# Kernel optimization log

Hardware: AMD Instinct MI355X
Metric: run time of the kernel (lower is better)

## Reference

```python
import jax, jax.numpy as jnp
import numpy as np

SEQ, B, IN, H = 512, 64, 256, 512

def _lin_params(key, out_d, in_d):
    k1, k2 = jax.random.split(key)
    bound = 1.0 / np.sqrt(in_d)
    w = jax.random.uniform(k1, (out_d, in_d), jnp.float32, -bound, bound)
    b = jax.random.uniform(k2, (out_d,), jnp.float32, -bound, bound)
    return w, b

def setup_inputs() -> dict:
    key = jax.random.key(0)
    ks = jax.random.split(key, 9)
    x = jax.random.normal(ks[0], (SEQ, B, IN), jnp.float32)
    h0 = jnp.zeros((B, H), jnp.float32)
    c0 = jnp.zeros((B, H), jnp.float32)
    Wf_w, Wf_b = _lin_params(ks[1], H, IN)
    Uf_w, Uf_b = _lin_params(ks[2], H, H)
    Wi_w, Wi_b = _lin_params(ks[3], H, IN)
    Ui_w, Ui_b = _lin_params(ks[4], H, H)
    Wo_w, Wo_b = _lin_params(ks[5], H, IN)
    Uo_w, Uo_b = _lin_params(ks[6], H, H)
    Wc_w, Wc_b = _lin_params(ks[7], H, IN)
    Uc_w, Uc_b = _lin_params(ks[8], H, H)
    return dict(x=x, h0=h0, c0=c0,
                Wf_w=Wf_w, Wf_b=Wf_b, Uf_w=Uf_w, Uf_b=Uf_b,
                Wi_w=Wi_w, Wi_b=Wi_b, Ui_w=Ui_w, Ui_b=Ui_b,
                Wo_w=Wo_w, Wo_b=Wo_b, Uo_w=Uo_w, Uo_b=Uo_b,
                Wc_w=Wc_w, Wc_b=Wc_b, Uc_w=Uc_w, Uc_b=Uc_b)

def reference(x, h0, c0,
              Wf_w, Wf_b, Uf_w, Uf_b,
              Wi_w, Wi_b, Ui_w, Ui_b,
              Wo_w, Wo_b, Uo_w, Uo_b,
              Wc_w, Wc_b, Uc_w, Uc_b):
    # Precompute all input-to-hidden projections in one batched GEMM per gate.
    xf = jnp.einsum('tbi,hi->tbh', x, Wf_w) + Wf_b  # (T,B,H)
    xi = jnp.einsum('tbi,hi->tbh', x, Wi_w) + Wi_b
    xo = jnp.einsum('tbi,hi->tbh', x, Wo_w) + Wo_b
    xc = jnp.einsum('tbi,hi->tbh', x, Wc_w) + Wc_b

    def step(carry, xs):
        h, c = carry
        xft, xit, xot, xct = xs
        f = jax.nn.sigmoid(xft + h @ Uf_w.T + Uf_b)
        i = jax.nn.sigmoid(xit + h @ Ui_w.T + Ui_b)
        o = jax.nn.sigmoid(xot + h @ Uo_w.T + Uo_b)
        c = f * c + i * jnp.tanh(xct + h @ Uc_w.T + Uc_b)
        h = o * jnp.tanh(c)
        return (h, c), h

    (h, c), h_seq = jax.lax.scan(step, (h0, c0), (xf, xi, xo, xc))
    return h_seq, h, c
```

## Files before the change

### kernel.cpp

```cpp
#include <hip/hip_runtime.h>


#define T_STEPS 512
#define BATCH   64
#define IN_D    256
#define HID     512
#define NGROUP  4
#define NSLICE  16
#define BLK_B   16
#define BLK_H   32
#define THREADS 512

using short8  = __attribute__((ext_vector_type(8))) short;
using float4v = __attribute__((ext_vector_type(4))) float;

#define FRAG_ADDR(f) (((f) << 4) + (((f) >> 4) << 4))

__device__ __forceinline__ unsigned short f2bf(float f) {
    union { float f; unsigned int i; } v; v.f = f;
    unsigned int r = v.i + 0x7fff + ((v.i >> 16) & 1);
    return (unsigned short)(r >> 16);
}
__device__ __forceinline__ short8 pack8(float4 a, float4 b) {
    short8 s;
    s[0]=(short)f2bf(a.x); s[1]=(short)f2bf(a.y); s[2]=(short)f2bf(a.z); s[3]=(short)f2bf(a.w);
    s[4]=(short)f2bf(b.x); s[5]=(short)f2bf(b.y); s[6]=(short)f2bf(b.z); s[7]=(short)f2bf(b.w);
    return s;
}
__device__ __forceinline__ float sigm(float v) { return 1.0f / (1.0f + __expf(-v)); }
__device__ __forceinline__ float tanh_(float v) { return 2.0f / (1.0f + __expf(-2.0f * v)) - 1.0f; }

__global__ __launch_bounds__(256, 1) void lstm_init_flags(unsigned int* flags, int n) {
    int i = blockIdx.x * blockDim.x + threadIdx.x;
    if (i < n) flags[i] = 0u;
}

__global__ __launch_bounds__(THREADS, 2) void lstm_persist(
    const float* __restrict__ x,
    const float* __restrict__ h0,
    const float* __restrict__ c0,
    const float* __restrict__ Wf, const float* __restrict__ Wfb,
    const float* __restrict__ Uf, const float* __restrict__ Ufb,
    const float* __restrict__ Wi, const float* __restrict__ Wib,
    const float* __restrict__ Ui, const float* __restrict__ Uib,
    const float* __restrict__ Wo, const float* __restrict__ Wob,
    const float* __restrict__ Uo, const float* __restrict__ Uob,
    const float* __restrict__ Wc, const float* __restrict__ Wcb,
    const float* __restrict__ Uc, const float* __restrict__ Ucb,
    float* out,
    unsigned int* flags)
{
    __shared__ __attribute__((aligned(16))) unsigned char hfrag[17392];
    __shared__ __attribute__((aligned(16))) unsigned char xfrag[8688];
    __shared__ float g_lds[8 * 256];

    const int tid  = threadIdx.x;
    const int lane = tid & 63;
    const int wave = tid >> 6;
    const int gate = wave >> 1;
    const int hlf  = wave & 1;
    const int grp  = blockIdx.x & 3;
    const int slc  = blockIdx.x >> 2;
    const int bb   = grp * BLK_B;
    const int hbase= slc * BLK_H;
    const int lm   = lane & 15;
    const int lq   = lane >> 4;
    const int row  = tid >> 5;
    const int seg  = tid & 31;

    const float* Ug  = (gate == 0) ? Uf : (gate == 1) ? Ui : (gate == 2) ? Uo : Uc;
    const float* Wg  = (gate == 0) ? Wf : (gate == 1) ? Wi : (gate == 2) ? Wo : Wc;
    const float* Wbg = (gate == 0) ? Wfb : (gate == 1) ? Wib : (gate == 2) ? Wob : Wcb;
    const float* Ubg = (gate == 0) ? Ufb : (gate == 1) ? Uib : (gate == 2) ? Uob : Ucb;
    const int ng = hbase + hlf * 16 + lm;

    short8 ufrag[16];
#pragma unroll
    for (int ks = 0; ks < 16; ++ks) {
        const float* p = Ug + (size_t)ng * HID + ks * 32 + lq * 8;
        ufrag[ks] = pack8(*(const float4*)(p), *(const float4*)(p + 4));
    }
    short8 wfrag[8];
#pragma unroll
    for (int ks = 0; ks < 8; ++ks) {
        const float* p = Wg + (size_t)ng * IN_D + ks * 32 + lq * 8;
        wfrag[ks] = pack8(*(const float4*)(p), *(const float4*)(p + 4));
    }
    const float bias = Wbg[ng] + Ubg[ng];

    float c_reg = c0[(size_t)(bb + row) * HID + hbase + seg];

    {
        const float* ph = h0 + (size_t)(bb + row) * HID + seg * 16;
        int f0 = (seg >> 1) * 64 + (seg & 1) * 32 + row;
        *(short8*)(hfrag + FRAG_ADDR(f0))      = pack8(*(const float4*)(ph),     *(const float4*)(ph + 4));
        *(short8*)(hfrag + FRAG_ADDR(f0 + 16)) = pack8(*(const float4*)(ph + 8), *(const float4*)(ph + 12));

        const float* px = x + (size_t)(bb + row) * IN_D + seg * 8;
        int fx = (seg >> 2) * 64 + (seg & 3) * 16 + row;
        *(short8*)(xfrag + FRAG_ADDR(fx)) = pack8(*(const float4*)(px), *(const float4*)(px + 4));
    }
    float4 xn0, xn1;
    {
        const float* px = x + ((size_t)1 * BATCH + bb + row) * IN_D + seg * 8;
        xn0 = *(const float4*)(px); xn1 = *(const float4*)(px + 4);
    }
    __syncthreads();

    float4v accx0 = {bias, bias, bias, bias};
    float4v accx1 = {0.f, 0.f, 0.f, 0.f};
#pragma unroll
    for (int ks = 0; ks < 8; ++ks) {
        short8 a = *(const short8*)(xfrag + FRAG_ADDR(ks * 64 + lane));
        if (ks & 1) accx1 = __builtin_amdgcn_mfma_f32_16x16x32_bf16(a, wfrag[ks], accx1, 0, 0, 0);
        else        accx0 = __builtin_amdgcn_mfma_f32_16x16x32_bf16(a, wfrag[ks], accx0, 0, 0, 0);
    }

    unsigned int* const cnt = flags + (size_t)grp * T_STEPS;
    float* const out_h = out + (size_t)T_STEPS * BATCH * HID;
    float* const out_c = out_h + (size_t)BATCH * HID;

    for (int t = 0; t < T_STEPS; ++t) {
        float4v acc0 = accx0, acc1 = accx1;
#pragma unroll
        for (int ks = 0; ks < 16; ++ks) {
            short8 a = *(const short8*)(hfrag + FRAG_ADDR(ks * 64 + lane));
            if (ks & 1) acc1 = __builtin_amdgcn_mfma_f32_16x16x32_bf16(a, ufrag[ks], acc1, 0, 0, 0);
            else        acc0 = __builtin_amdgcn_mfma_f32_16x16x32_bf16(a, ufrag[ks], acc0, 0, 0, 0);
        }
        float4v acc = acc0 + acc1;
#pragma unroll
        for (int r = 0; r < 4; ++r)
            g_lds[wave * 256 + (lq * 4 + r) * 16 + lm] = acc[r];
        __syncthreads();

        float hv;
        {
            int hf2 = seg >> 4, nn = seg & 15;
            float fpre = g_lds[(0 * 2 + hf2) * 256 + row * 16 + nn];
            float ipre = g_lds[(1 * 2 + hf2) * 256 + row * 16 + nn];
            float opre = g_lds[(2 * 2 + hf2) * 256 + row * 16 + nn];
            float gpre = g_lds[(3 * 2 + hf2) * 256 + row * 16 + nn];
            float fv = sigm(fpre), iv = sigm(ipre), ov = sigm(opre);
            float gv = tanh_(gpre);
            c_reg = fv * c_reg + iv * gv;
            hv = ov * tanh_(c_reg);
        }
        __hip_atomic_store(out + ((size_t)t * BATCH + bb + row) * HID + hbase + seg,
                           hv, __ATOMIC_RELAXED, __HIP_MEMORY_SCOPE_AGENT);
        if (t == T_STEPS - 1) {
            out_h[(size_t)(bb + row) * HID + hbase + seg] = hv;
            out_c[(size_t)(bb + row) * HID + hbase + seg] = c_reg;
        }

        if (t + 1 < T_STEPS) {
            int fx = (seg >> 2) * 64 + (seg & 3) * 16 + row;
            *(short8*)(xfrag + FRAG_ADDR(fx)) = pack8(xn0, xn1);
            int tn = (t + 2 < T_STEPS) ? (t + 2) : (T_STEPS - 1);
            const float* px = x + ((size_t)tn * BATCH + bb + row) * IN_D + seg * 8;
            xn0 = *(const float4*)(px); xn1 = *(const float4*)(px + 4);
        }

        asm volatile("s_waitcnt vmcnt(0)" ::: "memory");
        __syncthreads();

        if (t + 1 < T_STEPS) {
            if (tid == 0)
                __hip_atomic_fetch_add(&cnt[t], 1u, __ATOMIC_RELAXED, __HIP_MEMORY_SCOPE_AGENT);

            accx0 = (float4v){bias, bias, bias, bias};
            accx1 = (float4v){0.f, 0.f, 0.f, 0.f};
#pragma unroll
            for (int ks = 0; ks < 8; ++ks) {
                short8 a = *(const short8*)(xfrag + FRAG_ADDR(ks * 64 + lane));
                if (ks & 1) accx1 = __builtin_amdgcn_mfma_f32_16x16x32_bf16(a, wfrag[ks], accx1, 0, 0, 0);
                else        accx0 = __builtin_amdgcn_mfma_f32_16x16x32_bf16(a, wfrag[ks], accx0, 0, 0, 0);
            }

            if (tid == 0) {
                while (__hip_atomic_load(&cnt[t], __ATOMIC_RELAXED, __HIP_MEMORY_SCOPE_AGENT)
                       < (unsigned)NSLICE) {  }
            }
            __syncthreads();

            {
                const float* src = out + ((size_t)t * BATCH + bb + row) * HID + seg * 16;
                float4 a0 = *(const float4*)(src);
                float4 a1 = *(const float4*)(src + 4);
                float4 a2 = *(const float4*)(src + 8);
                float4 a3 = *(const float4*)(src + 12);
                int f0 = (seg >> 1) * 64 + (seg & 1) * 32 + row;
                *(short8*)(hfrag + FRAG_ADDR(f0))      = pack8(a0, a1);
                *(short8*)(hfrag + FRAG_ADDR(f0 + 16)) = pack8(a2, a3);
            }
            __syncthreads();
        }
    }
}

extern "C" void kernel_launch(void* const* d_in, const int* in_sizes, int n_in,
                              void* d_out, int out_size, void* d_ws, size_t ws_size,
                              hipStream_t stream) {
    (void)in_sizes; (void)n_in; (void)out_size; (void)ws_size;
    const float* x   = (const float*)d_in[0];
    const float* h0  = (const float*)d_in[1];
    const float* c0  = (const float*)d_in[2];
    const float* Wf  = (const float*)d_in[3];
    const float* Wfb = (const float*)d_in[4];
    const float* Uf  = (const float*)d_in[5];
    const float* Ufb = (const float*)d_in[6];
    const float* Wi  = (const float*)d_in[7];
    const float* Wib = (const float*)d_in[8];
    const float* Ui  = (const float*)d_in[9];
    const float* Uib = (const float*)d_in[10];
    const float* Wo  = (const float*)d_in[11];
    const float* Wob = (const float*)d_in[12];
    const float* Uo  = (const float*)d_in[13];
    const float* Uob = (const float*)d_in[14];
    const float* Wc  = (const float*)d_in[15];
    const float* Wcb = (const float*)d_in[16];
    const float* Uc  = (const float*)d_in[17];
    const float* Ucb = (const float*)d_in[18];

    unsigned int* flags = (unsigned int*)d_ws;
    const int nflags = NGROUP * T_STEPS;

    lstm_init_flags<<<(nflags + 255) / 256, 256, 0, stream>>>(flags, nflags);
    lstm_persist<<<NGROUP * NSLICE, THREADS, 0, stream>>>(
        x, h0, c0,
        Wf, Wfb, Uf, Ufb, Wi, Wib, Ui, Uib,
        Wo, Wob, Uo, Uob, Wc, Wcb, Uc, Ucb,
        (float*)d_out, flags);
}
```

Before: 1.570 ms.

## Replace counter barrier with flag-embedded bf16 hidden-state exchange buffer

Replaces the per-step atomic counter plus global re-read of fp32 h with a double-buffered exchange area. Each 16-byte chunk carries packed bf16 h values together with a step tag, so consumers poll their own data directly with system-coherent loads, dropping the fetch-add, the single-thread spin, and extra block barriers. Also moves the x prefetch and xfrag write earlier and uses lighter LDS-only barriers. Risks include relying on 16-byte store atomicity for tag/data consistency and a bounded spin guard that could silently break out early and read stale data.

```diff
diff --git a/kernel.cpp b/kernel.cpp
--- a/kernel.cpp
+++ b/kernel.cpp
@@ -10,8 +10,12 @@
 #define BLK_B   16
 #define BLK_H   32
 #define THREADS 512
+#define CH_ROW  128
+#define SLOT_BYTES (NGROUP * BLK_B * CH_ROW * 16)
+#define EXCH_INTS  (2 * SLOT_BYTES / 4)
 
 using short8  = __attribute__((ext_vector_type(8))) short;
+using int4v   = __attribute__((ext_vector_type(4))) int;
 using float4v = __attribute__((ext_vector_type(4))) float;
 
 #define FRAG_ADDR(f) (((f) << 4) + (((f) >> 4) << 4))
@@ -30,12 +34,18 @@
 __device__ __forceinline__ float sigm(float v) { return 1.0f / (1.0f + __expf(-v)); }
 __device__ __forceinline__ float tanh_(float v) { return 2.0f / (1.0f + __expf(-2.0f * v)) - 1.0f; }
 
-__global__ __launch_bounds__(256, 1) void lstm_init_flags(unsigned int* flags, int n) {
+__device__ __forceinline__ void lds_barrier() {
+    asm volatile("s_waitcnt lgkmcnt(0)" ::: "memory");
+    __builtin_amdgcn_s_barrier();
+    __builtin_amdgcn_sched_barrier(0);
+}
+
+__global__ __launch_bounds__(256, 1) void lstm_init_ws(unsigned int* w, int n) {
     int i = blockIdx.x * blockDim.x + threadIdx.x;
-    if (i < n) flags[i] = 0u;
-}
-
-__global__ __launch_bounds__(THREADS, 2) void lstm_persist(
+    if (i < n) __hip_atomic_store(&w[i], 0u, __ATOMIC_RELAXED, __HIP_MEMORY_SCOPE_AGENT);
+}
+
+__global__ __launch_bounds__(THREADS, 1) void lstm_persist(
     const float* __restrict__ x,
     const float* __restrict__ h0,
     const float* __restrict__ c0,
@@ -48,7 +58,7 @@
     const float* __restrict__ Wc, const float* __restrict__ Wcb,
     const float* __restrict__ Uc, const float* __restrict__ Ucb,
     float* out,
-    unsigned int* flags)
+    unsigned char* exch)
 {
     __shared__ __attribute__((aligned(16))) unsigned char hfrag[17392];
     __shared__ __attribute__((aligned(16))) unsigned char xfrag[8688];
@@ -116,11 +126,22 @@
         else        accx0 = __builtin_amdgcn_mfma_f32_16x16x32_bf16(a, wfrag[ks], accx0, 0, 0, 0);
     }
 
-    unsigned int* const cnt = flags + (size_t)grp * T_STEPS;
     float* const out_h = out + (size_t)T_STEPS * BATCH * HID;
     float* const out_c = out_h + (size_t)BATCH * HID;
 
+    unsigned char* const ex_wr = exch
+        + (size_t)((grp * BLK_B + row) * CH_ROW + slc * 8 + (seg >> 2)) * 16;
+    unsigned char* const ex_rd = exch
+        + (size_t)((grp * BLK_B + row) * CH_ROW + seg * 4) * 16;
+
     for (int t = 0; t < T_STEPS; ++t) {
+        float4 xm0, xm1;
+        {
+            int tn = (t + 2 < T_STEPS) ? (t + 2) : (T_STEPS - 1);
+            const float* px = x + ((size_t)tn * BATCH + bb + row) * IN_D + seg * 8;
+            xm0 = *(const float4*)(px); xm1 = *(const float4*)(px + 4);
+        }
+
         float4v acc0 = accx0, acc1 = accx1;
 #pragma unroll
         for (int ks = 0; ks < 16; ++ks) {
@@ -132,7 +153,14 @@
 #pragma unroll
         for (int r = 0; r < 4; ++r)
             g_lds[wave * 256 + (lq * 4 + r) * 16 + lm] = acc[r];
-        __syncthreads();
+
+        if (t + 1 < T_STEPS) {
+            int fx = (seg >> 2) * 64 + (seg & 3) * 16 + row;
+            *(short8*)(xfrag + FRAG_ADDR(fx)) = pack8(xn0, xn1);
+            xn0 = xm0; xn1 = xm1;
+        }
+
+        lds_barrier();
 
         float hv;
         {
@@ -146,27 +174,21 @@
             c_reg = fv * c_reg + iv * gv;
             hv = ov * tanh_(c_reg);
         }
-        __hip_atomic_store(out + ((size_t)t * BATCH + bb + row) * HID + hbase + seg,
-                           hv, __ATOMIC_RELAXED, __HIP_MEMORY_SCOPE_AGENT);
-        if (t == T_STEPS - 1) {
-            out_h[(size_t)(bb + row) * HID + hbase + seg] = hv;
-            out_c[(size_t)(bb + row) * HID + hbase + seg] = c_reg;
-        }
+        out[((size_t)t * BATCH + bb + row) * HID + hbase + seg] = hv;
 
         if (t + 1 < T_STEPS) {
-            int fx = (seg >> 2) * 64 + (seg & 3) * 16 + row;
-            *(short8*)(xfrag + FRAG_ADDR(fx)) = pack8(xn0, xn1);
-            int tn = (t + 2 < T_STEPS) ? (t + 2) : (T_STEPS - 1);
-            const float* px = x + ((size_t)tn * BATCH + bb + row) * IN_D + seg * 8;
-            xn0 = *(const float4*)(px); xn1 = *(const float4*)(px + 4);
-        }
-
-        asm volatile("s_waitcnt vmcnt(0)" ::: "memory");
-        __syncthreads();
-
-        if (t + 1 < T_STEPS) {
-            if (tid == 0)
-                __hip_atomic_fetch_add(&cnt[t], 1u, __ATOMIC_RELAXED, __HIP_MEMORY_SCOPE_AGENT);
+            {
+                unsigned int bfv = f2bf(hv);
+                unsigned int nb  = (unsigned int)__shfl_xor((int)bfv, 1);
+                unsigned int p   = bfv | (nb << 16);
+                unsigned int q   = (unsigned int)__shfl_xor((int)p, 2);
+                if ((lane & 3) == 0) {
+                    int4v ch; ch[0] = (int)p; ch[1] = (int)q; ch[2] = t + 1; ch[3] = 0;
+                    const unsigned char* pa = ex_wr + (size_t)(t & 1) * SLOT_BYTES;
+                    asm volatile("global_store_dwordx4 %0, %1, off sc0 sc1"
+                                 :: "v"(pa), "v"(ch) : "memory");
+                }
+            }
 
             accx0 = (float4v){bias, bias, bias, bias};
             accx1 = (float4v){0.f, 0.f, 0.f, 0.f};
@@ -177,23 +199,32 @@
                 else        accx0 = __builtin_amdgcn_mfma_f32_16x16x32_bf16(a, wfrag[ks], accx0, 0, 0, 0);
             }
 
-            if (tid == 0) {
-                while (__hip_atomic_load(&cnt[t], __ATOMIC_RELAXED, __HIP_MEMORY_SCOPE_AGENT)
-                       < (unsigned)NSLICE) {  }
+            const unsigned char* pb = ex_rd + (size_t)(t & 1) * SLOT_BYTES;
+            const int want = t + 1;
+            int4v e0, e1, e2, e3;
+            int guard = 0;
+            for (;;) {
+                asm volatile(
+                    "global_load_dwordx4 %0, %4, off sc0 sc1\n\t"
+                    "global_load_dwordx4 %1, %4, off offset:16 sc0 sc1\n\t"
+                    "global_load_dwordx4 %2, %4, off offset:32 sc0 sc1\n\t"
+                    "global_load_dwordx4 %3, %4, off offset:48 sc0 sc1\n\t"
+                    "s_waitcnt vmcnt(0)"
+                    : "=&v"(e0), "=&v"(e1), "=&v"(e2), "=&v"(e3)
+                    : "v"(pb) : "memory");
+                if ((e0[2] == want) & (e1[2] == want) & (e2[2] == want) & (e3[2] == want)) break;
+                if (++guard > (1 << 20)) break;
             }
-            __syncthreads();
-
-            {
-                const float* src = out + ((size_t)t * BATCH + bb + row) * HID + seg * 16;
-                float4 a0 = *(const float4*)(src);
-                float4 a1 = *(const float4*)(src + 4);
-                float4 a2 = *(const float4*)(src + 8);
-                float4 a3 = *(const float4*)(src + 12);
-                int f0 = (seg >> 1) * 64 + (seg & 1) * 32 + row;
-                *(short8*)(hfrag + FRAG_ADDR(f0))      = pack8(a0, a1);
-                *(short8*)(hfrag + FRAG_ADDR(f0 + 16)) = pack8(a2, a3);
-            }
-            __syncthreads();
+            int f0 = (seg >> 1) * 64 + (seg & 1) * 32 + row;
+            int4v d0 = {e0[0], e0[1], e1[0], e1[1]};
+            int4v d1 = {e2[0], e2[1], e3[0], e3[1]};
+            *(int4v*)(hfrag + FRAG_ADDR(f0))      = d0;
+            *(int4v*)(hfrag + FRAG_ADDR(f0 + 16)) = d1;
+
+            lds_barrier();
+        } else {
+            out_h[(size_t)(bb + row) * HID + hbase + seg] = hv;
+            out_c[(size_t)(bb + row) * HID + hbase + seg] = c_reg;
         }
     }
 }
@@ -222,13 +253,11 @@
     const float* Uc  = (const float*)d_in[17];
     const float* Ucb = (const float*)d_in[18];
 
-    unsigned int* flags = (unsigned int*)d_ws;
-    const int nflags = NGROUP * T_STEPS;
-
-    lstm_init_flags<<<(nflags + 255) / 256, 256, 0, stream>>>(flags, nflags);
+    unsigned int* ws = (unsigned int*)d_ws;
+    lstm_init_ws<<<(EXCH_INTS + 255) / 256, 256, 0, stream>>>(ws, EXCH_INTS);
     lstm_persist<<<NGROUP * NSLICE, THREADS, 0, stream>>>(
         x, h0, c0,
         Wf, Wfb, Uf, Ufb, Wi, Wib, Ui, Uib,
         Wo, Wob, Uo, Uob, Wc, Wcb, Uc, Ucb,
-        (float*)d_out, flags);
-}
+        (float*)d_out, (unsigned char*)d_ws);
+}
```

After: 1.785 ms. 1.14x slower.
